# Optimization experiments

Measured on AMD Instinct MI355X. Metric: run time of the kernel, lower is better.

The kernel has to match this reference:

```python
import jax, jax.numpy as jnp
import numpy as np

L, B, H, IN = 2, 32, 2048, 2048  # layers, batch, hidden, input (=hidden here)


def setup_inputs() -> dict:
    key = jax.random.key(0)
    ks = jax.random.split(key, 8)
    s = 0.02
    return {
        "h0": jax.random.normal(ks[0], (L, B, H), jnp.float32),
        "c0": jax.random.normal(ks[1], (L, B, H), jnp.float32),
        "W_ih": jax.random.normal(ks[2], (L, 4 * H, IN), jnp.float32) * s,
        "W_hh": jax.random.normal(ks[3], (L, 4 * H, H), jnp.float32) * s,
        "b_ih": jax.random.normal(ks[4], (L, 4 * H), jnp.float32) * s,
        "b_hh": jax.random.normal(ks[5], (L, 4 * H), jnp.float32) * s,
        "W_out": jax.random.normal(ks[6], (IN, H), jnp.float32) * s,
        "b_out": jax.random.normal(ks[7], (IN,), jnp.float32) * s,
        "seq_len": 128,
    }


def _lstm_cell(x, h, c, W_ih, W_hh, b_ih, b_hh):
    # gates: [B, 4H]; PyTorch LSTMCell gate order i, f, g, o
    gates = x @ W_ih.T + b_ih + h @ W_hh.T + b_hh
    i, f, g, o = jnp.split(gates, 4, axis=-1)
    c_new = jax.nn.sigmoid(f) * c + jax.nn.sigmoid(i) * jnp.tanh(g)
    h_new = jax.nn.sigmoid(o) * jnp.tanh(c_new)
    return h_new, c_new


def reference(h0, c0, W_ih, W_hh, b_ih, b_hh, W_out, b_out, seq_len):
    batch, hidden = h0.shape[1], h0.shape[2]
    x0 = jnp.zeros((batch, hidden), h0.dtype)

    def step(carry, _):
        x, h, c = carry  # h, c: [L, B, H]
        hs, cs = [], []
        inp = x
        for l in range(h.shape[0]):  # small fixed layer loop
            h_l, c_l = _lstm_cell(inp, h[l], c[l], W_ih[l], W_hh[l], b_ih[l], b_hh[l])
            hs.append(h_l)
            cs.append(c_l)
            inp = h_l
        last_h = hs[-1]
        x_next = last_h @ W_out.T + b_out  # projected feedback
        return (x_next, jnp.stack(hs), jnp.stack(cs)), last_h

    _, out_feats = jax.lax.scan(step, (x0, h0, c0), None, length=seq_len)
    return out_feats  # [seq_len, B, H] (stacked list of per-step top-layer h)
```

## Files before the change

### kernel.cpp

```cpp
#include <hip/hip_runtime.h>


typedef __attribute__((ext_vector_type(8))) short short8;
typedef __attribute__((ext_vector_type(4))) short short4v;
typedef __attribute__((ext_vector_type(4))) float f32x4;
typedef __attribute__((ext_vector_type(4))) unsigned int u32x4;

#define MFMA16(a, b, c) __builtin_amdgcn_mfma_f32_16x16x32_bf16((a), (b), (c), 0, 0, 0)

static constexpr int BATCH = 32;
static constexpr int HID = 2048;
static constexpr int NWG = 256;
static constexpr int NTHR = 512;
static constexpr int BH = BATCH * HID;
static constexpr size_t WMAT = (size_t)8192 * 2048;
static constexpr int LDS_RED_OFF = 139264;
static constexpr int LDS_BYTES = 155648;

#define AT_ADD(p, v) __hip_atomic_fetch_add((p), (v), __ATOMIC_RELAXED, __HIP_MEMORY_SCOPE_AGENT)
#define AT_LD(p) __hip_atomic_load((p), __ATOMIC_RELAXED, __HIP_MEMORY_SCOPE_AGENT)
#define AT_ST(p, v) __hip_atomic_store((p), (v), __ATOMIC_RELAXED, __HIP_MEMORY_SCOPE_AGENT)

__device__ __forceinline__ unsigned short f2bf(float x) {
  unsigned u = __float_as_uint(x);
  u += 0x7FFFu + ((u >> 16) & 1u);
  return (unsigned short)(u >> 16);
}
__device__ __forceinline__ float sigm(float x) { return 1.f / (1.f + __expf(-x)); }
__device__ __forceinline__ float tanh_(float x) {
  float e = __expf(2.f * x);
  return 1.f - 2.f / (e + 1.f);
}

__global__ void cvt_bf16_k(const float* __restrict__ s, unsigned short* __restrict__ d,
                           long n4) {
  long i = blockIdx.x * (long)blockDim.x + threadIdx.x;
  long st = (long)gridDim.x * blockDim.x;
  for (; i < n4; i += st) {
    float4 v = ((const float4*)s)[i];
    short4v o;
    o.x = (short)f2bf(v.x); o.y = (short)f2bf(v.y);
    o.z = (short)f2bf(v.z); o.w = (short)f2bf(v.w);
    ((short4v*)d)[i] = o;
  }
}

__global__ void tcvt_k(const float* __restrict__ src, unsigned short* __restrict__ dst) {
  __shared__ float T[64][65];
  const int jb = blockIdx.x * 64, kb = blockIdx.y * 64;
  const int tid = threadIdx.x;
#pragma unroll
  for (int r = 0; r < 4; ++r) {
    const int row = r * 16 + (tid >> 4), c4 = (tid & 15) * 4;
    float4 v = *(const float4*)&src[(size_t)(jb + row) * 2048 + kb + c4];
    T[row][c4] = v.x; T[row][c4 + 1] = v.y; T[row][c4 + 2] = v.z; T[row][c4 + 3] = v.w;
  }
  __syncthreads();
#pragma unroll
  for (int r = 0; r < 4; ++r) {
    const int k = r * 16 + (tid >> 4), j4 = (tid & 15) * 4;
    short4v o;
    o.x = (short)f2bf(T[j4][k]);     o.y = (short)f2bf(T[j4 + 1][k]);
    o.z = (short)f2bf(T[j4 + 2][k]); o.w = (short)f2bf(T[j4 + 3][k]);
    *(short4v*)&dst[(size_t)(kb + k) * 2048 + jb + j4] = o;
  }
}

__global__ void gemm_pack_k(const unsigned short* __restrict__ A,
                            const unsigned short* __restrict__ Bt,
                            unsigned short* __restrict__ Wfp) {
  __shared__ __align__(16) unsigned short As[128][72], Bs[128][72];
  const int tid = threadIdx.x, wv = tid >> 6, lane = tid & 63;
  const int wm = wv >> 1, wn = wv & 1;
  const int g0 = blockIdx.x * 128, k0 = blockIdx.y * 128;
  f32x4 acc[4][4];
#pragma unroll
  for (int i = 0; i < 4; ++i)
#pragma unroll
    for (int j = 0; j < 4; ++j) acc[i][j] = (f32x4){0.f, 0.f, 0.f, 0.f};

  for (int kt = 0; kt < 32; ++kt) {
#pragma unroll
    for (int rr = 0; rr < 4; ++rr) {
      const int row = rr * 32 + (tid >> 3), c8 = (tid & 7) * 8;
      *(short8*)&As[row][c8] = *(const short8*)&A[(size_t)(g0 + row) * 2048 + kt * 64 + c8];
      *(short8*)&Bs[row][c8] = *(const short8*)&Bt[(size_t)(k0 + row) * 2048 + kt * 64 + c8];
    }
    __syncthreads();
#pragma unroll
    for (int kk = 0; kk < 2; ++kk) {
      short8 af[4], bf[4];
#pragma unroll
      for (int mi = 0; mi < 4; ++mi)
        af[mi] = *(const short8*)&As[wm * 64 + mi * 16 + (lane & 15)][kk * 32 + (lane >> 4) * 8];
#pragma unroll
      for (int ni = 0; ni < 4; ++ni)
        bf[ni] = *(const short8*)&Bs[wn * 64 + ni * 16 + (lane & 15)][kk * 32 + (lane >> 4) * 8];
#pragma unroll
      for (int mi = 0; mi < 4; ++mi)
#pragma unroll
        for (int ni = 0; ni < 4; ++ni)
          acc[mi][ni] = MFMA16(af[mi], bf[ni], acc[mi][ni]);
    }
    __syncthreads();
  }
#pragma unroll
  for (int mi = 0; mi < 4; ++mi)
#pragma unroll
    for (int ni = 0; ni < 4; ++ni)
#pragma unroll
      for (int r = 0; r < 4; ++r) {
        const int g = g0 + wm * 64 + mi * 16 + (lane >> 4) * 4 + r;
        const int k = k0 + wn * 64 + ni * 16 + (lane & 15);
        const int gateblk = g >> 11, gcol = g & 2047;
        const int wgp = gcol >> 3, nn = (gcol & 7) + 8 * (gateblk & 1), tile = gateblk >> 1;
        const int kblk = k >> 5, e = k & 7, lane_p = nn + 16 * ((k >> 3) & 3);
        Wfp[(((size_t)(wgp * 2 + tile) * 64 + kblk) * 64 + lane_p) * 8 + e] =
            f2bf(acc[mi][ni][r]);
      }
}

__global__ void pack_W1_k(const float* __restrict__ src, unsigned short* __restrict__ dst) {
  const int bid = blockIdx.x;
  const int wg = bid >> 1, tile = bid & 1;
  const int tid = threadIdx.x;
  __shared__ __align__(16) unsigned short L[16][2056];
  for (int i = tid; i < 16 * 512; i += 256) {
    const int r = i >> 9, c4 = i & 511;
    const int gr = tile * 4096 + (r < 8 ? wg * 8 + r : 2048 + wg * 8 + r - 8);
    float4 v = ((const float4*)(src + (size_t)gr * 2048))[c4];
    short4v o;
    o.x = (short)f2bf(v.x); o.y = (short)f2bf(v.y);
    o.z = (short)f2bf(v.z); o.w = (short)f2bf(v.w);
    *(short4v*)&L[r][c4 * 4] = o;
  }
  __syncthreads();
  short8* dchunks = (short8*)dst;
  const size_t cbase = (size_t)(wg * 2 + tile) * 64;
  for (int c = tid; c < 4096; c += 256) {
    const int lane = c & 63, kblk = c >> 6;
    const int nn = lane & 15, kb = (lane >> 4) << 3;
    short8 v = *(const short8*)&L[nn][kblk * 32 + kb];
    dchunks[(cbase + kblk) * 64 + lane] = v;
  }
}

__global__ void bias_k(const float* __restrict__ Wih, const float* __restrict__ bout,
                       const float* __restrict__ bih, const float* __restrict__ bhh,
                       float* bA0, float* bAf, float* bB) {
  const int g = blockIdx.x * 8 + (threadIdx.x >> 6);
  const int lane = threadIdx.x & 63;
  float s = 0.f;
  for (int i = 0; i < 32; ++i)
    s += Wih[(size_t)g * 2048 + i * 64 + lane] * bout[i * 64 + lane];
  for (int off = 32; off; off >>= 1) s += __shfl_down(s, off);
  if (lane == 0) {
    const float b0 = bih[g] + bhh[g];
    bA0[g] = b0; bAf[g] = b0 + s;
    bB[g] = bih[8192 + g] + bhh[8192 + g];
  }
}

__global__ void init_k(const float* __restrict__ h0, const float* __restrict__ c0,
                       unsigned short* hX, unsigned short* zbuf,
                       float* c0f, float* c1f, unsigned* ctl) {
  int i = blockIdx.x * blockDim.x + threadIdx.x;
  if (i < BH) {
    const int e = i & 7, lane = (i >> 3) & 63, kblk = (i >> 9) & 63, mtile = i >> 15;
    const int m = mtile * 16 + (lane & 15);
    const int k = kblk * 32 + ((lane >> 4) << 3) + e;
    const unsigned short v0 = f2bf(h0[m * HID + k]);
    const unsigned short v1 = f2bf(h0[BH + m * HID + k]);
#pragma unroll
    for (int x = 0; x < 8; ++x) {
      hX[(size_t)x * 131072 + i] = v0;
      hX[(size_t)x * 131072 + 65536 + i] = v1;
    }
    zbuf[i] = 0;
    c0f[i] = c0[i];
    c1f[i] = c0[BH + i];
  }
  if (i < 832) ctl[i] = 0u;
}

__device__ __forceinline__ void phase_sync(unsigned* ctl, int bno, int lbno, int xcc,
                                           int role, int n_x, int n_c, int w, int lane,
                                           const unsigned short* hGm,
                                           unsigned short* Xm) {
  asm volatile("s_waitcnt vmcnt(0)" ::: "memory");
  __syncthreads();
  if (threadIdx.x == 0) {
    const int g = blockIdx.x >> 5;
    unsigned a = AT_ADD(&ctl[g * 32], 1u);
    if (a == (unsigned)(32 * bno - 1)) {
      unsigned m = AT_ADD(&ctl[256], 1u);
      if (m == (unsigned)(8 * bno - 1)) AT_ST(&ctl[288], (unsigned)bno);
    }
    while (AT_LD(&ctl[288]) < (unsigned)bno) __builtin_amdgcn_s_sleep(1);
  }
  __syncthreads();
  asm volatile("buffer_inv" ::: "memory");
  if (role < n_c) {
    for (int c = role * 8 + w; c < 128; c += n_c * 8) {
      const unsigned short* s = hGm + c * 512 + lane * 8;
      u32x4 v;
      asm volatile("global_load_dwordx4 %0, %1, off sc0 sc1"
                   : "=v"(v) : "v"((unsigned long long)(size_t)s) : "memory");
      asm volatile("s_waitcnt vmcnt(0)" ::: "memory");
      *(u32x4*)(Xm + c * 512 + lane * 8) = v;
    }
  }
  asm volatile("s_waitcnt vmcnt(0)" ::: "memory");
  __syncthreads();
  if (threadIdx.x == 0) {
    AT_ADD(&ctl[320 + xcc * 32], 1u);
    while (AT_LD(&ctl[320 + xcc * 32]) < (unsigned)(n_x * lbno))
      __builtin_amdgcn_s_sleep(1);
  }
  __syncthreads();
  asm volatile("buffer_inv" ::: "memory");
}

#define PHASE_BODY(VARR, NV2, LBASE, CBUF, HOUTP, OUTP, BSEL)                     \
  {                                                                               \
    const short8* pa0 = (const short8*)Asrc + (size_t)(ks * 16) * 64 + lane;      \
    const short8* pa1 = pa0 + (size_t)64 * 64;                                    \
    f32x4 acc00 = {0.f, 0.f, 0.f, 0.f}, acc01 = acc00, acc10 = acc00, acc11 = acc00; \
    _Pragma("unroll")                                                             \
    for (int kk = 0; kk < NV2; ++kk) {                                            \
      short8 a0 = pa0[kk * 64], a1 = pa1[kk * 64];                                \
      short8 b0 = VARR[kk], b1 = VARR[16 + kk];                                   \
      acc00 = MFMA16(a0, b0, acc00); acc01 = MFMA16(a1, b0, acc01);               \
      acc10 = MFMA16(a0, b1, acc10); acc11 = MFMA16(a1, b1, acc11);               \
    }                                                                             \
    _Pragma("unroll")                                                             \
    for (int kk = NV2; kk < 16; ++kk) {                                           \
      short8 a0 = pa0[kk * 64], a1 = pa1[kk * 64];                                \
      short8 b0 = VARR[kk];                                                       \
      short8 b1 = lw[(w * 17 + LBASE + (kk - NV2)) * 64 + lane];                  \
      acc00 = MFMA16(a0, b0, acc00); acc01 = MFMA16(a1, b0, acc01);               \
      acc10 = MFMA16(a0, b1, acc10); acc11 = MFMA16(a1, b1, acc11);               \
    }                                                                             \
    *(f32x4*)&red[((w * 2 + 0) * 64 + lane) * 4] = acc00;                         \
    *(f32x4*)&red[((w * 2 + 1) * 64 + lane) * 4] = acc01;                         \
    __syncthreads();                                                              \
    float gi = 0.f, gf_ = 0.f;                                                    \
    if (tid < 256) {                                                              \
      const int b = tid >> 3, cc = tid & 7, m = b >> 4, br = b & 15;              \
      const int reg = br & 3, lb = (br >> 2) << 4;                                \
      _Pragma("unroll")                                                           \
      for (int ww = 0; ww < 8; ++ww) {                                            \
        gi  += red[((ww * 2 + m) * 64 + lb + cc) * 4 + reg];                      \
        gf_ += red[((ww * 2 + m) * 64 + lb + cc + 8) * 4 + reg];                  \
      }                                                                           \
    }                                                                             \
    __syncthreads();                                                              \
    *(f32x4*)&red[((w * 2 + 0) * 64 + lane) * 4] = acc10;                         \
    *(f32x4*)&red[((w * 2 + 1) * 64 + lane) * 4] = acc11;                         \
    __syncthreads();                                                              \
    if (tid < 256) {                                                              \
      const int b = tid >> 3, cc = tid & 7, m = b >> 4, br = b & 15;              \
      const int reg = br & 3, lb = (br >> 2) << 4;                                \
      float gg = 0.f, go = 0.f;                                                   \
      _Pragma("unroll")                                                           \
      for (int ww = 0; ww < 8; ++ww) {                                            \
        gg += red[((ww * 2 + m) * 64 + lb + cc) * 4 + reg];                       \
        go += red[((ww * 2 + m) * 64 + lb + cc + 8) * 4 + reg];                   \
      }                                                                           \
      const int col = wg * 8 + cc;                                                \
      gi  += (BSEL)[col];                                                         \
      gf_ += (BSEL)[2048 + col];                                                  \
      gg  += (BSEL)[4096 + col];                                                  \
      go  += (BSEL)[6144 + col];                                                  \
      const float iv = sigm(gi), fv = sigm(gf_), gv = tanh_(gg), ov = sigm(go);   \
      const float cold = (CBUF)[b * HID + col];                                   \
      const float cnew = fv * cold + iv * gv;                                     \
      const float hnew = ov * tanh_(cnew);                                        \
      (CBUF)[b * HID + col] = cnew;                                               \
      const int kblk = col >> 5, lh = (col >> 3) & 3, e = col & 7;                \
      const int lane_p = (b & 15) | (lh << 4), mt = b >> 4;                       \
      const unsigned hv = (unsigned)f2bf(hnew);                                   \
      unsigned long long ha = (unsigned long long)(size_t)                        \
          ((HOUTP) + ((size_t)(mt * 64 + kblk) * 64 + lane_p) * 8 + e);           \
      asm volatile("global_store_short %0, %1, off sc0 sc1"                       \
                   :: "v"(ha), "v"(hv) : "memory");                               \
      if (OUTP) ((float*)(OUTP))[b * HID + col] = hnew;                           \
    }                                                                             \
  }

__global__ __launch_bounds__(NTHR, 1) void lstm_persist(
    const unsigned short* __restrict__ Wfp, const unsigned short* __restrict__ Wh0p,
    const unsigned short* __restrict__ Wi1p, const unsigned short* __restrict__ Wh1p,
    const float* __restrict__ bA0, const float* __restrict__ bAf,
    const float* __restrict__ bB,
    unsigned short* hX,
    unsigned short* hG,
    const unsigned short* zbuf,
    float* c0f, float* c1f, float* __restrict__ out, int T, unsigned* ctl) {
  extern __shared__ __align__(16) char smem[];
  short8* lw = (short8*)smem;
  float* red = (float*)(smem + LDS_RED_OFF);
  const int wg = blockIdx.x, tid = threadIdx.x;
  const int w = tid >> 6, lane = tid & 63, ks = w & 3;
  const int xcc = (int)(__builtin_amdgcn_s_getreg((20) | (0 << 6) | (31 << 11)) & 7);
  const unsigned short* M0 = (w < 4) ? Wfp : Wh0p;
  const unsigned short* M1 = (w < 4) ? Wi1p : Wh1p;

  if (tid == 0) *(int*)red = (int)AT_ADD(&ctl[576 + xcc * 32], 1u);

  short8 v0[24], v1[23];
  {
    const short8* m0c = (const short8*)M0;
    const short8* m1c = (const short8*)M1;
#pragma unroll
    for (int c = 0; c < 24; ++c)
      v0[c] = m0c[(((size_t)(wg * 2 + (c >> 4)) * 64) + ks * 16 + (c & 15)) * 64 + lane];
#pragma unroll
    for (int c = 24; c < 32; ++c)
      lw[(w * 17 + (c - 24)) * 64 + lane] =
          m0c[(((size_t)(wg * 2 + (c >> 4)) * 64) + ks * 16 + (c & 15)) * 64 + lane];
#pragma unroll
    for (int c = 0; c < 23; ++c)
      v1[c] = m1c[(((size_t)(wg * 2 + (c >> 4)) * 64) + ks * 16 + (c & 15)) * 64 + lane];
#pragma unroll
    for (int c = 23; c < 32; ++c)
      lw[(w * 17 + 8 + (c - 23)) * 64 + lane] =
          m1c[(((size_t)(wg * 2 + (c >> 4)) * 64) + ks * 16 + (c & 15)) * 64 + lane];
  }
  __syncthreads();
  const int role = *(int*)red;
  unsigned short* Xh0 = hX + (size_t)xcc * 131072;
  unsigned short* Xh1 = Xh0 + 65536;

  asm volatile("s_waitcnt vmcnt(0)" ::: "memory");
  __syncthreads();
  if (tid == 0) {
    const int g = blockIdx.x >> 5;
    unsigned a = AT_ADD(&ctl[g * 32], 1u);
    if (a == 31u) {
      unsigned m = AT_ADD(&ctl[256], 1u);
      if (m == 7u) AT_ST(&ctl[288], 1u);
    }
    while (AT_LD(&ctl[288]) < 1u) __builtin_amdgcn_s_sleep(1);
    *(int*)red = (int)AT_LD(&ctl[576 + xcc * 32]);
  }
  __syncthreads();
  const int n_x = *(int*)red;
  const int n_c = n_x < 16 ? n_x : 16;
  __syncthreads();

  int bno = 2, lbno = 1;
  for (int t = 0; t < T; ++t) {
    {
      const unsigned short* Asrc = (w < 4) ? ((t == 0) ? zbuf : Xh1) : Xh0;
      const float* bsel = (t == 0) ? bA0 : bAf;
      PHASE_BODY(v0, 8, 0, c0f, hG, (float*)nullptr, bsel)
    }
    phase_sync(ctl, bno++, lbno++, xcc, role, n_x, n_c, w, lane, hG, Xh0);
    {
      const unsigned short* Asrc = (w < 4) ? Xh0 : Xh1;
      PHASE_BODY(v1, 7, 8, c1f, hG + 65536, out + (size_t)t * BH, bB)
    }
    phase_sync(ctl, bno++, lbno++, xcc, role, n_x, n_c, w, lane, hG + 65536, Xh1);
  }
}

extern "C" void kernel_launch(void* const* d_in, const int* in_sizes, int n_in,
                              void* d_out, int out_size, void* d_ws, size_t ws_size,
                              hipStream_t stream) {
  const float* h0 = (const float*)d_in[0];
  const float* c0 = (const float*)d_in[1];
  const float* Wih = (const float*)d_in[2];
  const float* Whh = (const float*)d_in[3];
  const float* bih = (const float*)d_in[4];
  const float* bhh = (const float*)d_in[5];
  const float* Wout = (const float*)d_in[6];
  const float* bout = (const float*)d_in[7];
  float* out = (float*)d_out;
  const int T = out_size / BH;

  unsigned short* Wfp = (unsigned short*)d_ws;
  unsigned short* Wh0p = Wfp + WMAT;
  unsigned short* Wi1p = Wfp + 2 * WMAT;
  unsigned short* Wh1p = Wfp + 3 * WMAT;
  unsigned short* tmpA = Wi1p;
  unsigned short* WoutT = Wh1p;
  unsigned short* S = Wfp + 4 * WMAT;
  unsigned short* hX = S;
  unsigned short* hG = S + 1048576;
  unsigned short* zbuf = S + 1179648;
  float* F = (float*)(S + 1245184);
  float* c0f = F;
  float* c1f = F + 65536;
  float* bA0 = F + 131072;
  float* bAf = F + 139264;
  float* bB = F + 147456;
  unsigned* ctl = (unsigned*)(F + 155648);

  cvt_bf16_k<<<2048, 256, 0, stream>>>(Wih, tmpA, (long)(WMAT / 4));
  tcvt_k<<<dim3(32, 32), 256, 0, stream>>>(Wout, WoutT);
  gemm_pack_k<<<dim3(64, 16), 256, 0, stream>>>(tmpA, WoutT, Wfp);
  pack_W1_k<<<512, 256, 0, stream>>>(Whh, Wh0p);
  pack_W1_k<<<512, 256, 0, stream>>>(Wih + WMAT, Wi1p);
  pack_W1_k<<<512, 256, 0, stream>>>(Whh + WMAT, Wh1p);
  bias_k<<<1024, 512, 0, stream>>>(Wih, bout, bih, bhh, bA0, bAf, bB);
  init_k<<<256, 256, 0, stream>>>(h0, c0, hX, zbuf, c0f, c1f, ctl);

  (void)hipFuncSetAttribute((const void*)lstm_persist,
                            hipFuncAttributeMaxDynamicSharedMemorySize, LDS_BYTES);
  lstm_persist<<<NWG, NTHR, LDS_BYTES, stream>>>(Wfp, Wh0p, Wi1p, Wh1p,
                                                 bA0, bAf, bB,
                                                 hX, hG, zbuf, c0f, c1f, out, T, ctl);
}
```

Baseline: 3.682 ms.

## Software-pipeline activation loads with manual vmcnt waits and drop buffer_inv

Replaces compiler-generated activation loads in the phase body with hand-issued global loads into a 4-deep register ring, interleaved with MFMAs and guarded by explicit vmcnt waits, so load latency overlaps compute. Loads use the sc0 cache bit. Also removes the buffer_inv cache invalidations after the grid barriers in phase_sync. This relies on the cache bits alone to keep cross-workgroup data fresh, which risks reading stale data if coherence is not otherwise ensured.

```diff
diff --git a/kernel.cpp b/kernel.cpp
--- a/kernel.cpp
+++ b/kernel.cpp
@@ -20,6 +20,9 @@
 #define AT_ADD(p, v) __hip_atomic_fetch_add((p), (v), __ATOMIC_RELAXED, __HIP_MEMORY_SCOPE_AGENT)
 #define AT_LD(p) __hip_atomic_load((p), __ATOMIC_RELAXED, __HIP_MEMORY_SCOPE_AGENT)
 #define AT_ST(p, v) __hip_atomic_store((p), (v), __ATOMIC_RELAXED, __HIP_MEMORY_SCOPE_AGENT)
+
+#define GLA(dst, ab) \
+  asm volatile("global_load_dwordx4 %0, %1, off sc0" : "=v"(dst) : "v"(ab) : "memory")
 
 __device__ __forceinline__ unsigned short f2bf(float x) {
   unsigned u = __float_as_uint(x);
@@ -199,7 +202,6 @@
     while (AT_LD(&ctl[288]) < (unsigned)bno) __builtin_amdgcn_s_sleep(1);
   }
   __syncthreads();
-  asm volatile("buffer_inv" ::: "memory");
   if (role < n_c) {
     for (int c = role * 8 + w; c < 128; c += n_c * 8) {
       const unsigned short* s = hGm + c * 512 + lane * 8;
@@ -218,28 +220,38 @@
       __builtin_amdgcn_s_sleep(1);
   }
   __syncthreads();
-  asm volatile("buffer_inv" ::: "memory");
 }
 
 #define PHASE_BODY(VARR, NV2, LBASE, CBUF, HOUTP, OUTP, BSEL)                     \
   {                                                                               \
-    const short8* pa0 = (const short8*)Asrc + (size_t)(ks * 16) * 64 + lane;      \
-    const short8* pa1 = pa0 + (size_t)64 * 64;                                    \
+    const unsigned long long a0b = (unsigned long long)(size_t)Asrc +             \
+        ((unsigned long long)(ks * 16 * 64 + lane)) * 16ull;                      \
+    const unsigned long long a1b = a0b + 65536ull;                                \
+    short8 S0[4], S1[4];                                                          \
+    _Pragma("unroll")                                                             \
+    for (int p = 0; p < 4; ++p) {                                                 \
+      GLA(S0[p], a0b + (unsigned long long)p * 1024ull);                          \
+      GLA(S1[p], a1b + (unsigned long long)p * 1024ull);                          \
+    }                                                                             \
     f32x4 acc00 = {0.f, 0.f, 0.f, 0.f}, acc01 = acc00, acc10 = acc00, acc11 = acc00; \
     _Pragma("unroll")                                                             \
-    for (int kk = 0; kk < NV2; ++kk) {                                            \
-      short8 a0 = pa0[kk * 64], a1 = pa1[kk * 64];                                \
-      short8 b0 = VARR[kk], b1 = VARR[16 + kk];                                   \
-      acc00 = MFMA16(a0, b0, acc00); acc01 = MFMA16(a1, b0, acc01);               \
-      acc10 = MFMA16(a0, b1, acc10); acc11 = MFMA16(a1, b1, acc11);               \
-    }                                                                             \
-    _Pragma("unroll")                                                             \
-    for (int kk = NV2; kk < 16; ++kk) {                                           \
-      short8 a0 = pa0[kk * 64], a1 = pa1[kk * 64];                                \
+    for (int kk = 0; kk < 16; ++kk) {                                             \
+      if (kk < 13) { asm volatile("s_waitcnt vmcnt(6)" ::: "memory"); }           \
+      else if (kk == 13) { asm volatile("s_waitcnt vmcnt(4)" ::: "memory"); }     \
+      else if (kk == 14) { asm volatile("s_waitcnt vmcnt(2)" ::: "memory"); }     \
+      else { asm volatile("s_waitcnt vmcnt(0)" ::: "memory"); }                   \
+      __builtin_amdgcn_sched_barrier(0);                                          \
       short8 b0 = VARR[kk];                                                       \
-      short8 b1 = lw[(w * 17 + LBASE + (kk - NV2)) * 64 + lane];                  \
-      acc00 = MFMA16(a0, b0, acc00); acc01 = MFMA16(a1, b0, acc01);               \
-      acc10 = MFMA16(a0, b1, acc10); acc11 = MFMA16(a1, b1, acc11);               \
+      short8 b1 = (kk < NV2) ? VARR[16 + kk]                                      \
+                             : lw[(w * 17 + LBASE + (kk - NV2)) * 64 + lane];     \
+      acc00 = MFMA16(S0[kk & 3], b0, acc00);                                      \
+      acc01 = MFMA16(S1[kk & 3], b0, acc01);                                      \
+      acc10 = MFMA16(S0[kk & 3], b1, acc10);                                      \
+      acc11 = MFMA16(S1[kk & 3], b1, acc11);                                      \
+      if (kk < 12) {                                                              \
+        GLA(S0[kk & 3], a0b + (unsigned long long)(kk + 4) * 1024ull);            \
+        GLA(S1[kk & 3], a1b + (unsigned long long)(kk + 4) * 1024ull);            \
+      }                                                                           \
     }                                                                             \
     *(f32x4*)&red[((w * 2 + 0) * 64 + lane) * 4] = acc00;                         \
     *(f32x4*)&red[((w * 2 + 1) * 64 + lane) * 4] = acc01;                         \
```

Result: slower. 3.806 ms (+3.4%).
